# Kernel tuning notes

Hardware: AMD Instinct MI355X
Metric: run time of the kernel (lower is better)

## Reference

```python
import jax, jax.numpy as jnp
import numpy as np

DT = 1e-3  # integration step (coeffs[3])
B, T = 512, 8192


def setup_inputs() -> dict:
    key = jax.random.key(0)
    k1, k2, k3, k4 = jax.random.split(key, 4)
    xicovs = jax.random.normal(k1, (B, T, 2, 2), dtype=jnp.float32) * 0.1
    dy = jax.random.normal(k2, (B, T, 2), dtype=jnp.float32) * 0.1
    # learned 2x2 kernel (initializer='uniform' in keras -> small uniform)
    coeffs_A = jax.random.uniform(k3, (2, 2), minval=-0.05, maxval=0.05, dtype=jnp.float32)
    # fixed measurement matrix C (coeffs[0])
    C = jnp.array([[0.5, 0.1], [-0.1, 0.5]], dtype=jnp.float32)
    del k4
    return {"xicovs": xicovs, "dy": dy, "coeffs_A": coeffs_A, "C": C}


def reference(xicovs, dy, coeffs_A, C):
    # xicovs: [B,T,2,2], dy: [B,T,2], coeffs_A/C: [2,2]
    b = xicovs.shape[0]
    x0 = jnp.tile(jnp.array([[1.0, 0.0]], dtype=xicovs.dtype), (b, 1))  # initial_state
    xic_tm = jnp.transpose(xicovs, (1, 0, 2, 3))  # [T,B,2,2] time-major
    dy_tm = jnp.transpose(dy, (1, 0, 2))          # [T,B,2]

    def step(x, inp):
        xic, dyt = inp
        # A - xicov @ C, per batch element
        A_mx = coeffs_A - jnp.einsum('bij,jk->bik', xic, C)
        out = jnp.einsum('ij,bj->bi', C, x) * DT          # emitted output uses prev state
        dx = jnp.einsum('bij,bj->bi', A_mx, x) * DT + jnp.einsum('bij,bj->bi', xic, dyt)
        return x + dx, out

    _, outs = jax.lax.scan(step, x0, (xic_tm, dy_tm))  # outs: [T,B,2]
    return jnp.transpose(outs, (1, 0, 2))  # [B,T,2] (return_sequences=True)
```

## Files before the change

### kernel.cpp

```cpp
#include <hip/hip_runtime.h>

namespace {

constexpr float kDT = 1e-3f;
constexpr int kB = 512;
constexpr int kT = 8192;
constexpr int kThreads = 1024;
constexpr int kSteps = kT / kThreads;
constexpr int kWaves = kThreads / 64;

struct Xf { float a, b, c, d, p, q; };

__device__ __forceinline__ Xf comp(const Xf& e, const Xf& l) {
  Xf o;
  o.a = l.a * e.a + l.b * e.c;
  o.b = l.a * e.b + l.b * e.d;
  o.c = l.c * e.a + l.d * e.c;
  o.d = l.c * e.b + l.d * e.d;
  o.p = l.a * e.p + l.b * e.q + l.p;
  o.q = l.c * e.p + l.d * e.q + l.q;
  return o;
}

__device__ __forceinline__ Xf shfl_up_xf(const Xf& v, int d) {
  Xf r;
  r.a = __shfl_up(v.a, d);
  r.b = __shfl_up(v.b, d);
  r.c = __shfl_up(v.c, d);
  r.d = __shfl_up(v.d, d);
  r.p = __shfl_up(v.p, d);
  r.q = __shfl_up(v.q, d);
  return r;
}

__global__ __launch_bounds__(kThreads) void k_fused(
    const float* __restrict__ xic, const float* __restrict__ dy,
    const float* __restrict__ Ap, const float* __restrict__ Cp,
    float* __restrict__ out) {
  __shared__ float sWT[kWaves][6];
  __shared__ float sWE[kWaves][6];

  const int tid = threadIdx.x;
  const int lane = tid & 63;
  const int w = tid >> 6;
  const size_t base = (size_t)blockIdx.x * kT + (size_t)tid * kSteps;

  const float A00 = Ap[0], A01 = Ap[1], A10 = Ap[2], A11 = Ap[3];
  const float C00 = Cp[0], C01 = Cp[1], C10 = Cp[2], C11 = Cp[3];

  float4 xv[kSteps];
  float2 dv[kSteps];
#pragma unroll
  for (int k = 0; k < kSteps; ++k) {
    xv[k] = reinterpret_cast<const float4*>(xic)[base + k];
    dv[k] = reinterpret_cast<const float2*>(dy)[base + k];
  }

  float m0[kSteps], m1[kSteps], m2[kSteps], m3[kSteps], m4[kSteps], m5[kSteps];
#pragma unroll
  for (int k = 0; k < kSteps; ++k) {
    m0[k] = 1.0f + kDT * (A00 - (xv[k].x * C00 + xv[k].y * C10));
    m1[k] =        kDT * (A01 - (xv[k].x * C01 + xv[k].y * C11));
    m2[k] =        kDT * (A10 - (xv[k].z * C00 + xv[k].w * C10));
    m3[k] = 1.0f + kDT * (A11 - (xv[k].z * C01 + xv[k].w * C11));
    m4[k] = xv[k].x * dv[k].x + xv[k].y * dv[k].y;
    m5[k] = xv[k].z * dv[k].x + xv[k].w * dv[k].y;
  }

  Xf tot{m0[0], m1[0], m2[0], m3[0], m4[0], m5[0]};
#pragma unroll
  for (int k = 1; k < kSteps; ++k) {
    const Xf s{m0[k], m1[k], m2[k], m3[k], m4[k], m5[k]};
    tot = comp(tot, s);
  }

  Xf inc = tot;
#pragma unroll
  for (int d = 1; d < 64; d <<= 1) {
    const Xf r = shfl_up_xf(inc, d);
    if (lane >= d) inc = comp(r, inc);
  }

  if (lane == 63) {
    sWT[w][0] = inc.a; sWT[w][1] = inc.b; sWT[w][2] = inc.c;
    sWT[w][3] = inc.d; sWT[w][4] = inc.p; sWT[w][5] = inc.q;
  }
  __syncthreads();

  if (tid == 0) {
    Xf pre{1.f, 0.f, 0.f, 1.f, 0.f, 0.f};
    for (int i = 0; i < kWaves; ++i) {
      sWE[i][0] = pre.a; sWE[i][1] = pre.b; sWE[i][2] = pre.c;
      sWE[i][3] = pre.d; sWE[i][4] = pre.p; sWE[i][5] = pre.q;
      const Xf wt{sWT[i][0], sWT[i][1], sWT[i][2],
                  sWT[i][3], sWT[i][4], sWT[i][5]};
      pre = comp(pre, wt);
    }
  }
  __syncthreads();

  const Xf Ew{sWE[w][0], sWE[w][1], sWE[w][2],
              sWE[w][3], sWE[w][4], sWE[w][5]};

  Xf le = shfl_up_xf(inc, 1);
  if (lane == 0) le = Xf{1.f, 0.f, 0.f, 1.f, 0.f, 0.f};

  const Xf ex = comp(Ew, le);

  float x0 = ex.a + ex.p;
  float x1 = ex.c + ex.q;

#pragma unroll
  for (int k = 0; k < kSteps; ++k) {
    float2 o;
    o.x = kDT * (C00 * x0 + C01 * x1);
    o.y = kDT * (C10 * x0 + C11 * x1);
    reinterpret_cast<float2*>(out)[base + k] = o;
    const float nx0 = m0[k] * x0 + m1[k] * x1 + m4[k];
    const float nx1 = m2[k] * x0 + m3[k] * x1 + m5[k];
    x0 = nx0; x1 = nx1;
  }
}

}

extern "C" void kernel_launch(void* const* d_in, const int* in_sizes, int n_in,
                              void* d_out, int out_size, void* d_ws,
                              size_t ws_size, hipStream_t stream) {
  const float* xic = (const float*)d_in[0];
  const float* dy  = (const float*)d_in[1];
  const float* Ap  = (const float*)d_in[2];
  const float* Cp  = (const float*)d_in[3];
  float* out = (float*)d_out;

  k_fused<<<kB, kThreads, 0, stream>>>(xic, dy, Ap, Cp, out);
}
```

Measured before the change: 35.24 us.

## Restructure scan into coalesced multi-pass chunks with prefetch and parallel wave scan

Each thread now handles two adjacent timesteps per pass over 2048-step chunks, so global loads and stores become contiguous float4 accesses across the block. Before, each thread read eight consecutive steps, which made per-thread memory access strided. The next chunk's inputs are prefetched into registers while the current chunk is scanned. A carried state links the chunks. The serial thread-0 combination of wave totals is replaced with a shuffle-based scan in wave 0. The cost is four scan rounds and eight block barriers per row instead of one round and two barriers.

```diff
diff --git a/kernel.cpp b/kernel.cpp
--- a/kernel.cpp
+++ b/kernel.cpp
@@ -6,8 +6,9 @@
 constexpr int kB = 512;
 constexpr int kT = 8192;
 constexpr int kThreads = 1024;
-constexpr int kSteps = kT / kThreads;
 constexpr int kWaves = kThreads / 64;
+constexpr int kPassSteps = 2 * kThreads;
+constexpr int kPasses = kT / kPassSteps;
 
 struct Xf { float a, b, c, d, p, q; };
 
@@ -33,92 +34,124 @@
   return r;
 }
 
+__device__ __forceinline__ Xf make_xf(const float4 xv, float d0, float d1,
+                                      float A00, float A01, float A10, float A11,
+                                      float C00, float C01, float C10, float C11) {
+  Xf m;
+  m.a = 1.0f + kDT * (A00 - (xv.x * C00 + xv.y * C10));
+  m.b =        kDT * (A01 - (xv.x * C01 + xv.y * C11));
+  m.c =        kDT * (A10 - (xv.z * C00 + xv.w * C10));
+  m.d = 1.0f + kDT * (A11 - (xv.z * C01 + xv.w * C11));
+  m.p = xv.x * d0 + xv.y * d1;
+  m.q = xv.z * d0 + xv.w * d1;
+  return m;
+}
+
 __global__ __launch_bounds__(kThreads) void k_fused(
     const float* __restrict__ xic, const float* __restrict__ dy,
     const float* __restrict__ Ap, const float* __restrict__ Cp,
     float* __restrict__ out) {
   __shared__ float sWT[kWaves][6];
-  __shared__ float sWE[kWaves][6];
+  __shared__ float sWI[kWaves][6];
 
   const int tid = threadIdx.x;
   const int lane = tid & 63;
   const int w = tid >> 6;
-  const size_t base = (size_t)blockIdx.x * kT + (size_t)tid * kSteps;
+  const size_t rbase = (size_t)blockIdx.x * kT;
+  const size_t rbase2 = (size_t)blockIdx.x * (kT / 2);
+
+  const float4* X4 = reinterpret_cast<const float4*>(xic);
+  const float4* D4 = reinterpret_cast<const float4*>(dy);
+  float4* O4 = reinterpret_cast<float4*>(out);
 
   const float A00 = Ap[0], A01 = Ap[1], A10 = Ap[2], A11 = Ap[3];
   const float C00 = Cp[0], C01 = Cp[1], C10 = Cp[2], C11 = Cp[3];
 
-  float4 xv[kSteps];
-  float2 dv[kSteps];
-#pragma unroll
-  for (int k = 0; k < kSteps; ++k) {
-    xv[k] = reinterpret_cast<const float4*>(xic)[base + k];
-    dv[k] = reinterpret_cast<const float2*>(dy)[base + k];
+  float4 xva[2], xvb[2], dva[2];
+
+  {
+    const size_t s = (size_t)2 * tid;
+    xva[0] = X4[rbase + s];
+    xvb[0] = X4[rbase + s + 1];
+    dva[0] = D4[rbase2 + tid];
   }
 
-  float m0[kSteps], m1[kSteps], m2[kSteps], m3[kSteps], m4[kSteps], m5[kSteps];
-#pragma unroll
-  for (int k = 0; k < kSteps; ++k) {
-    m0[k] = 1.0f + kDT * (A00 - (xv[k].x * C00 + xv[k].y * C10));
-    m1[k] =        kDT * (A01 - (xv[k].x * C01 + xv[k].y * C11));
-    m2[k] =        kDT * (A10 - (xv[k].z * C00 + xv[k].w * C10));
-    m3[k] = 1.0f + kDT * (A11 - (xv[k].z * C01 + xv[k].w * C11));
-    m4[k] = xv[k].x * dv[k].x + xv[k].y * dv[k].y;
-    m5[k] = xv[k].z * dv[k].x + xv[k].w * dv[k].y;
-  }
-
-  Xf tot{m0[0], m1[0], m2[0], m3[0], m4[0], m5[0]};
-#pragma unroll
-  for (int k = 1; k < kSteps; ++k) {
-    const Xf s{m0[k], m1[k], m2[k], m3[k], m4[k], m5[k]};
-    tot = comp(tot, s);
-  }
-
-  Xf inc = tot;
-#pragma unroll
-  for (int d = 1; d < 64; d <<= 1) {
-    const Xf r = shfl_up_xf(inc, d);
-    if (lane >= d) inc = comp(r, inc);
-  }
-
-  if (lane == 63) {
-    sWT[w][0] = inc.a; sWT[w][1] = inc.b; sWT[w][2] = inc.c;
-    sWT[w][3] = inc.d; sWT[w][4] = inc.p; sWT[w][5] = inc.q;
-  }
-  __syncthreads();
-
-  if (tid == 0) {
-    Xf pre{1.f, 0.f, 0.f, 1.f, 0.f, 0.f};
-    for (int i = 0; i < kWaves; ++i) {
-      sWE[i][0] = pre.a; sWE[i][1] = pre.b; sWE[i][2] = pre.c;
-      sWE[i][3] = pre.d; sWE[i][4] = pre.p; sWE[i][5] = pre.q;
-      const Xf wt{sWT[i][0], sWT[i][1], sWT[i][2],
-                  sWT[i][3], sWT[i][4], sWT[i][5]};
-      pre = comp(pre, wt);
-    }
-  }
-  __syncthreads();
-
-  const Xf Ew{sWE[w][0], sWE[w][1], sWE[w][2],
-              sWE[w][3], sWE[w][4], sWE[w][5]};
-
-  Xf le = shfl_up_xf(inc, 1);
-  if (lane == 0) le = Xf{1.f, 0.f, 0.f, 1.f, 0.f, 0.f};
-
-  const Xf ex = comp(Ew, le);
-
-  float x0 = ex.a + ex.p;
-  float x1 = ex.c + ex.q;
+  float x0 = 1.0f, x1 = 0.0f;
 
 #pragma unroll
-  for (int k = 0; k < kSteps; ++k) {
-    float2 o;
-    o.x = kDT * (C00 * x0 + C01 * x1);
-    o.y = kDT * (C10 * x0 + C11 * x1);
-    reinterpret_cast<float2*>(out)[base + k] = o;
-    const float nx0 = m0[k] * x0 + m1[k] * x1 + m4[k];
-    const float nx1 = m2[k] * x0 + m3[k] * x1 + m5[k];
-    x0 = nx0; x1 = nx1;
+  for (int c = 0; c < kPasses; ++c) {
+    const int buf = c & 1;
+    if (c + 1 < kPasses) {
+      const size_t s = (size_t)(c + 1) * kPassSteps + 2 * tid;
+      xva[buf ^ 1] = X4[rbase + s];
+      xvb[buf ^ 1] = X4[rbase + s + 1];
+      dva[buf ^ 1] = D4[rbase2 + (size_t)(c + 1) * kThreads + tid];
+    }
+
+    const Xf s0 = make_xf(xva[buf], dva[buf].x, dva[buf].y,
+                          A00, A01, A10, A11, C00, C01, C10, C11);
+    const Xf s1 = make_xf(xvb[buf], dva[buf].z, dva[buf].w,
+                          A00, A01, A10, A11, C00, C01, C10, C11);
+    const Xf tot = comp(s0, s1);
+
+    Xf inc = tot;
+#pragma unroll
+    for (int d = 1; d < 64; d <<= 1) {
+      const Xf r = shfl_up_xf(inc, d);
+      if (lane >= d) inc = comp(r, inc);
+    }
+
+    if (lane == 63) {
+      sWT[w][0] = inc.a; sWT[w][1] = inc.b; sWT[w][2] = inc.c;
+      sWT[w][3] = inc.d; sWT[w][4] = inc.p; sWT[w][5] = inc.q;
+    }
+    __syncthreads();
+
+    if (w == 0) {
+      Xf v{1.f, 0.f, 0.f, 1.f, 0.f, 0.f};
+      if (lane < kWaves) {
+        v = Xf{sWT[lane][0], sWT[lane][1], sWT[lane][2],
+               sWT[lane][3], sWT[lane][4], sWT[lane][5]};
+      }
+#pragma unroll
+      for (int d = 1; d < kWaves; d <<= 1) {
+        const Xf r = shfl_up_xf(v, d);
+        if (lane >= d && lane < kWaves) v = comp(r, v);
+      }
+      if (lane < kWaves) {
+        sWI[lane][0] = v.a; sWI[lane][1] = v.b; sWI[lane][2] = v.c;
+        sWI[lane][3] = v.d; sWI[lane][4] = v.p; sWI[lane][5] = v.q;
+      }
+    }
+    __syncthreads();
+
+    Xf Ew{1.f, 0.f, 0.f, 1.f, 0.f, 0.f};
+    if (w > 0) {
+      Ew = Xf{sWI[w - 1][0], sWI[w - 1][1], sWI[w - 1][2],
+              sWI[w - 1][3], sWI[w - 1][4], sWI[w - 1][5]};
+    }
+    Xf le = shfl_up_xf(inc, 1);
+    if (lane == 0) le = Xf{1.f, 0.f, 0.f, 1.f, 0.f, 0.f};
+
+    const Xf ex = comp(Ew, le);
+
+    float e0 = ex.a * x0 + ex.b * x1 + ex.p;
+    float e1 = ex.c * x0 + ex.d * x1 + ex.q;
+
+    float4 o;
+    o.x = kDT * (C00 * e0 + C01 * e1);
+    o.y = kDT * (C10 * e0 + C11 * e1);
+    const float t0 = s0.a * e0 + s0.b * e1 + s0.p;
+    const float t1 = s0.c * e0 + s0.d * e1 + s0.q;
+    o.z = kDT * (C00 * t0 + C01 * t1);
+    o.w = kDT * (C10 * t0 + C11 * t1);
+    O4[rbase2 + (size_t)c * kThreads + tid] = o;
+
+    const Xf T{sWI[kWaves - 1][0], sWI[kWaves - 1][1], sWI[kWaves - 1][2],
+               sWI[kWaves - 1][3], sWI[kWaves - 1][4], sWI[kWaves - 1][5]};
+    const float n0 = T.a * x0 + T.b * x1 + T.p;
+    const float n1 = T.c * x0 + T.d * x1 + T.q;
+    x0 = n0; x1 = n1;
   }
 }
 
```

New measurement: 33.85 us. 3.9% less time.
